# Optimization experiments

Hardware: AMD Instinct MI355X
Metric: run time of the kernel (lower is better)

The kernel has to match this reference:

```python
import jax, jax.numpy as jnp
import numpy as np

B, T, C, D, P = 8, 512, 32, 128, 1024
EPS = 1e-5

def setup_inputs() -> dict:
    key = jax.random.key(0)
    ks = jax.random.split(key, 11)
    s = 1.0 / np.sqrt(D)
    inp = {
        'x': jax.random.normal(ks[0], (B, T, C, D), jnp.float32),
        'x_mask': jax.random.randint(ks[1], (B, T, C), 0, 2) == 1,
        'p_mask': jax.random.randint(ks[2], (B, T, C), 0, 2) == 1,
        'pos': jax.random.randint(ks[3], (B, T, C), 0, P),
        'pe': jax.random.normal(ks[4], (P, D // 2, 2), jnp.float32),  # complex rpe as [re, im]
        'imp': jax.random.randint(ks[5], (B, T), 0, C),
        'idx_c': jax.random.randint(ks[6], (B, T, C), 0, C),
        'wq_w': jax.random.normal(ks[7], (D, D), jnp.float32) * s,
        'wq_b': jnp.zeros((D,), jnp.float32),
        'wk_w': jax.random.normal(ks[8], (D, D), jnp.float32) * s,
        'wk_b': jnp.zeros((D,), jnp.float32),
        'wv_w': jax.random.normal(ks[9], (D, D), jnp.float32) * s,
        'wv_b': jnp.zeros((D,), jnp.float32),
        'ls_gamma': 1e-5 * jnp.ones((D,), jnp.float32),
        'ln_gamma': jnp.ones((D,), jnp.float32),
        'ln_beta': jnp.zeros((D,), jnp.float32),
    }
    return inp


def _rotate(z, r):
    # z: (b,t,c,d) real; r: (b,t,c,d/2,2) complex multiplier [re,im]
    b, t, c, d = z.shape
    zr = z.reshape(b, t, c, d // 2, 2)
    re = zr[..., 0] * r[..., 0] - zr[..., 1] * r[..., 1]
    im = zr[..., 0] * r[..., 1] + zr[..., 1] * r[..., 0]
    return jnp.stack([re, im], axis=-1).reshape(b, t, c, d)


def reference(x, x_mask, p_mask, pos, pe, imp, idx_c,
              wq_w, wq_b, wk_w, wk_b, wv_w, wv_b,
              ls_gamma, ln_gamma, ln_beta):
    b, t, c, d = x.shape
    # channel selection gather: where x_mask, use per-token important channel
    imp_rep = jnp.broadcast_to(imp[:, :, None], (b, t, c))
    idx = jnp.where(x_mask, imp_rep, idx_c)            # (b,t,c)
    xg = jnp.take_along_axis(x, idx[..., None], axis=2)  # (b,t,c,d)
    # QKV projections (torch Linear: x @ W.T + b)
    q = xg @ wq_w.T + wq_b
    k = xg @ wk_w.T + wk_b
    v = xg @ wv_w.T + wv_b
    # relative PE complex rotation on q,k
    r = pe[pos]                                        # (b,t,c,d/2,2)
    q = _rotate(q, r)
    k = _rotate(k, r)
    # (b,c,t,d) layout; channel acts as head
    qt = q.transpose(0, 2, 1, 3)
    kt = k.transpose(0, 2, 1, 3)
    vt = v.transpose(0, 2, 1, 3)
    scores = jnp.einsum('bcqd,bckd->bcqk', qt, kt) / jnp.sqrt(jnp.float32(d))
    pm = p_mask.transpose(0, 2, 1)                     # (b,c,t)
    mask = pm[:, :, :, None] | pm[:, :, None, :]       # (b,c,t,t)
    attn = jax.nn.softmax(jnp.where(mask, -jnp.inf, scores), axis=-1)
    attn = jnp.nan_to_num(attn)
    xm = x_mask.transpose(0, 2, 1)                     # (b,c,t)
    weight = jnp.where(xm, 1.0 / t, 1.0)
    out = jnp.einsum('bcmn,bcnd->bmcd', attn * weight[:, :, None, :], vt)  # (b,t,c,d)
    # norm_first=False: LN(x + layer_scale(out))
    y = x + ls_gamma * out
    mu = jnp.mean(y, axis=-1, keepdims=True)
    var = jnp.mean(jnp.square(y - mu), axis=-1, keepdims=True)
    return (y - mu) / jnp.sqrt(var + EPS) * ln_gamma + ln_beta
```

## Files before the change

kernel.cpp:

```cpp
#include <hip/hip_runtime.h>
#include <hip/hip_bf16.h>

#define Bb 8
#define Tt 512
#define Cc 32
#define Dd 128
#define SCALE 0.08838834764831845f
#define SROW 520

typedef unsigned int u32;
typedef __hip_bfloat16 bf16;
typedef __attribute__((ext_vector_type(8))) short short8;
typedef __attribute__((ext_vector_type(4))) short short4v;
typedef __attribute__((ext_vector_type(4))) float floatx4;

__device__ __forceinline__ short f2bf(float f) {
    __hip_bfloat16 h = __float2bfloat16(f);
    return *(short*)&h;
}
__device__ __forceinline__ float bf2f(short s) {
    return __uint_as_float(((u32)(unsigned short)s) << 16);
}

__global__ __launch_bounds__(256)
void k_wconv(const float* __restrict__ wq, const float* __restrict__ wk,
             const float* __restrict__ wv, short* __restrict__ Wb)
{
    int g = blockIdx.x * 256 + threadIdx.x;
    int mat = g >> 14, rem = g & 16383;
    const float* src = (mat == 0) ? wq : (mat == 1) ? wk : wv;
    Wb[g] = f2bf(src[rem]);
}

__global__ __launch_bounds__(256)
void k_qkvm(const float* __restrict__ x, const int* __restrict__ xm,
            const int* __restrict__ pos, const float* __restrict__ pe,
            const int* __restrict__ imp, const int* __restrict__ idxc,
            const short* __restrict__ Wb,
            const float* __restrict__ bq, const float* __restrict__ bk,
            const float* __restrict__ bv,
            short* __restrict__ qb, short* __restrict__ kb, short* __restrict__ vb)
{
    const int R0  = blockIdx.x * 64;
    const int b   = R0 >> 14;
    const int t0  = (R0 >> 5) & 511;
    const int tid = threadIdx.x;
    const int w    = tid >> 6;
    const int lane = tid & 63;
    const int quad = lane >> 4;
    const int m    = lane & 15;

    __shared__ short xg[64 * 136];
    __shared__ short ot[64 * 392];

#pragma unroll
    for (int i = 0; i < 8; ++i) {
        int u   = tid + i * 256;
        int row = u >> 5, seg = u & 31;
        int R   = R0 + row;
        int idx = xm[R] ? imp[R >> 5] : idxc[R];
        float4 v = *(const float4*)(x + ((long)(R >> 5) * Cc + idx) * Dd + seg * 4);
        short4v s = {f2bf(v.x), f2bf(v.y), f2bf(v.z), f2bf(v.w)};
        *(short4v*)&xg[row * 136 + seg * 4] = s;
    }

    short8 wf[6][4];
    float  bias_v[6];
#pragma unroll
    for (int mat = 0; mat < 3; ++mat) {
        const float* bp = (mat == 0) ? bq : (mat == 1) ? bk : bv;
#pragma unroll
        for (int h = 0; h < 2; ++h) {
            int sl = mat * 2 + h;
            int ct = h * 4 + w;
            bias_v[sl] = bp[ct * 16 + m];
#pragma unroll
            for (int kb = 0; kb < 4; ++kb)
                wf[sl][kb] = *(const short8*)(Wb + ((long)mat * 128 + ct * 16 + m) * 128
                                              + kb * 32 + quad * 8);
        }
    }
    __syncthreads();

    for (int rt = 0; rt < 4; ++rt) {
        short8 af[4];
#pragma unroll
        for (int kb = 0; kb < 4; ++kb)
            af[kb] = *(const short8*)&xg[(rt * 16 + m) * 136 + kb * 32 + quad * 8];

        floatx4 acc[6];
#pragma unroll
        for (int sl = 0; sl < 6; ++sl) acc[sl] = (floatx4){0.f, 0.f, 0.f, 0.f};
#pragma unroll
        for (int kb = 0; kb < 4; ++kb)
#pragma unroll
            for (int sl = 0; sl < 6; ++sl)
                acc[sl] = __builtin_amdgcn_mfma_f32_16x16x32_bf16(af[kb], wf[sl][kb], acc[sl], 0, 0, 0);

        int po[4];
#pragma unroll
        for (int r = 0; r < 4; ++r) po[r] = pos[R0 + rt * 16 + quad * 4 + r];

#pragma unroll
        for (int sl = 0; sl < 6; ++sl) {
            int mat = sl >> 1;
            int ct  = (sl & 1) * 4 + w;
            int d   = ct * 16 + m;
#pragma unroll
            for (int r = 0; r < 4; ++r) {
                float v = acc[sl][r] + bias_v[sl];
                float p = __shfl_xor(v, 1, 64);
                if (mat < 2) {
                    const float* rp = pe + ((long)po[r] * (Dd / 2) + (d >> 1)) * 2;
                    float r0 = rp[0], r1 = rp[1];
                    v = (d & 1) ? fmaf(p, r1, v * r0) : fmaf(v, r0, -(p * r1));
                    if (mat == 0) v *= SCALE;
                }
                ot[(rt * 16 + quad * 4 + r) * 392 + mat * 128 + d] = f2bf(v);
            }
        }
    }
    __syncthreads();

    short* const mats[3] = {qb, kb, vb};
#pragma unroll
    for (int mat = 0; mat < 3; ++mat) {
        short* dst = mats[mat];
#pragma unroll
        for (int i = 0; i < 4; ++i) {
            int g = tid + i * 256;
            int n = g >> 4, off = (g & 15) * 8;
            int c = n & 31, tl = n >> 5;
            *(short8*)(dst + (((long)(b * Cc + c) * Tt) + t0 + tl) * Dd + off) =
                *(const short8*)&ot[n * 392 + mat * 128 + off];
        }
    }
}

__global__ __launch_bounds__(256)
void k_vt(const short* __restrict__ vb, const int* __restrict__ xm,
          short* __restrict__ vt)
{
    const int head = blockIdx.y;
    const int b    = head >> 5;
    const int c    = head & 31;
    const int t0   = blockIdx.x * 64;
    const int tid  = threadIdx.x;

    __shared__ short tile[64 * 136];
    __shared__ float wks[64];

    if (tid < 64)
        wks[tid] = xm[((long)b * Tt + t0 + tid) * Cc + c] ? (1.0f / Tt) : 1.0f;

    const short* src = vb + ((long)head * Tt + t0) * Dd;
#pragma unroll
    for (int i = 0; i < 4; ++i) {
        int u = tid + i * 256;
        int row = u >> 4, col = (u & 15) * 8;
        *(short8*)&tile[row * 136 + col] = *(const short8*)(src + row * Dd + col);
    }
    __syncthreads();

    short* dst = vt + (long)head * Dd * Tt + t0;
#pragma unroll
    for (int i = 0; i < 4; ++i) {
        int u = tid + i * 256;
        int d = u >> 3, t8 = (u & 7) * 8;
        short8 v;
#pragma unroll
        for (int j = 0; j < 8; ++j)
            v[j] = f2bf(bf2f(tile[(t8 + j) * 136 + d]) * wks[t8 + j]);
        *(short8*)(dst + (long)d * Tt + t8) = v;
    }
}

__global__ __launch_bounds__(512, 4)
void k_attn(const short* __restrict__ qb, const short* __restrict__ kbp,
            const short* __restrict__ vtp, const float* __restrict__ x,
            const int* __restrict__ pm,
            const float* __restrict__ lsg, const float* __restrict__ lng,
            const float* __restrict__ lnb, float* __restrict__ out)
{
    const int head = blockIdx.x;
    const int b    = head >> 5;
    const int c    = head & 31;
    const int qt0  = blockIdx.y * 64;
    const int tid  = threadIdx.x;
    const int w    = tid >> 6;
    const int lane = tid & 63;
    const int quad = lane >> 4;
    const int m    = lane & 15;

    __shared__ short S[64 * SROW];
    __shared__ u32   pkbits[16];
    __shared__ float rlS[64];
    __shared__ float ps1[8][64];
    __shared__ float ps2[8][64];
    __shared__ float mrs[64][2];

    {
        bool v = pm[((long)b * Tt + tid) * Cc + c] != 0;
        unsigned long long bal = __ballot(v);
        if (lane == 0) {
            pkbits[w * 2]     = (u32)bal;
            pkbits[w * 2 + 1] = (u32)(bal >> 32);
        }
    }

    short8 qf[4][4];
#pragma unroll
    for (int qt = 0; qt < 4; ++qt)
#pragma unroll
        for (int kb = 0; kb < 4; ++kb)
            qf[qt][kb] = *(const short8*)(qb + ((long)head * Tt + qt0 + qt * 16 + m) * Dd
                                          + kb * 32 + quad * 8);
    __syncthreads();

    for (int ch = 0; ch < 4; ++ch) {
        int kt = ch * 128 + w * 16 + m;
        const short* kp = kbp + ((long)head * Tt + kt) * Dd + quad * 8;
        floatx4 sc[4];
#pragma unroll
        for (int qt = 0; qt < 4; ++qt) sc[qt] = (floatx4){0.f, 0.f, 0.f, 0.f};
#pragma unroll
        for (int kb = 0; kb < 4; ++kb) {
            short8 bk = *(const short8*)(kp + kb * 32);
#pragma unroll
            for (int qt = 0; qt < 4; ++qt)
                sc[qt] = __builtin_amdgcn_mfma_f32_16x16x32_bf16(qf[qt][kb], bk, sc[qt], 0, 0, 0);
        }
        bool masked = (pkbits[kt >> 5] >> (kt & 31)) & 1;
#pragma unroll
        for (int qt = 0; qt < 4; ++qt)
#pragma unroll
            for (int r = 0; r < 4; ++r)
                S[(qt * 16 + quad * 4 + r) * SROW + kt] = f2bf(masked ? -1e30f : sc[qt][r]);
    }
    __syncthreads();

    {
        int qi = tid >> 3, part = tid & 7;
        short* rowp = &S[qi * SROW + part * 64];
        short8 sv[8];
#pragma unroll
        for (int j = 0; j < 8; ++j) sv[j] = *(short8*)&rowp[j * 8];
        float mx = -1e30f;
#pragma unroll
        for (int j = 0; j < 8; ++j)
#pragma unroll
            for (int e = 0; e < 8; ++e) mx = fmaxf(mx, bf2f(sv[j][e]));
        mx = fmaxf(mx, __shfl_xor(mx, 1, 64));
        mx = fmaxf(mx, __shfl_xor(mx, 2, 64));
        mx = fmaxf(mx, __shfl_xor(mx, 4, 64));
        float l = 0.f;
#pragma unroll
        for (int j = 0; j < 8; ++j)
#pragma unroll
            for (int e = 0; e < 8; ++e) {
                float s = bf2f(sv[j][e]);
                float ex = (s <= -1e29f) ? 0.f : __expf(s - mx);
                sv[j][e] = f2bf(ex);
                l += ex;
            }
#pragma unroll
        for (int j = 0; j < 8; ++j) *(short8*)&rowp[j * 8] = sv[j];
        l += __shfl_xor(l, 1, 64);
        l += __shfl_xor(l, 2, 64);
        l += __shfl_xor(l, 4, 64);
        if (part == 0) {
            int t = qt0 + qi;
            bool qmask = (pkbits[t >> 5] >> (t & 31)) & 1;
            rlS[qi] = (l > 0.f && !qmask) ? 1.0f / l : 0.f;
        }
    }
    __syncthreads();

    floatx4 oa[4];
#pragma unroll
    for (int qt = 0; qt < 4; ++qt) oa[qt] = (floatx4){0.f, 0.f, 0.f, 0.f};

    const short* vbase = vtp + (long)head * Dd * Tt + ((long)(w * 16 + m)) * Tt + quad * 8;
    for (int kv = 0; kv < 16; ++kv) {
        short8 bv = *(const short8*)(vbase + kv * 32);
#pragma unroll
        for (int qt = 0; qt < 4; ++qt) {
            short8 ap = *(const short8*)&S[(qt * 16 + m) * SROW + kv * 32 + quad * 8];
            oa[qt] = __builtin_amdgcn_mfma_f32_16x16x32_bf16(ap, bv, oa[qt], 0, 0, 0);
        }
    }

    const int d = w * 16 + m;
    const float lg = lsg[d];
    float yv[4][4];
    float s1[4][4], s2[4][4];
#pragma unroll
    for (int qt = 0; qt < 4; ++qt)
#pragma unroll
        for (int r = 0; r < 4; ++r) {
            int row = qt * 16 + quad * 4 + r;
            int t = qt0 + row;
            float val = oa[qt][r] * rlS[row];
            float y = x[(((long)b * Tt + t) * Cc + c) * Dd + d] + lg * val;
            yv[qt][r] = y;
            s1[qt][r] = y;
            s2[qt][r] = y * y;
        }
#pragma unroll
    for (int qt = 0; qt < 4; ++qt)
#pragma unroll
        for (int r = 0; r < 4; ++r) {
            float a = s1[qt][r], bb = s2[qt][r];
            a += __shfl_xor(a, 1, 64); bb += __shfl_xor(bb, 1, 64);
            a += __shfl_xor(a, 2, 64); bb += __shfl_xor(bb, 2, 64);
            a += __shfl_xor(a, 4, 64); bb += __shfl_xor(bb, 4, 64);
            a += __shfl_xor(a, 8, 64); bb += __shfl_xor(bb, 8, 64);
            if (m == 0) {
                ps1[w][qt * 16 + quad * 4 + r] = a;
                ps2[w][qt * 16 + quad * 4 + r] = bb;
            }
        }
    __syncthreads();
    if (tid < 64) {
        float a = 0.f, bb = 0.f;
#pragma unroll
        for (int wv = 0; wv < 8; ++wv) { a += ps1[wv][tid]; bb += ps2[wv][tid]; }
        float mean = a * (1.0f / Dd);
        float var  = bb * (1.0f / Dd) - mean * mean;
        mrs[tid][0] = mean;
        mrs[tid][1] = rsqrtf(var + 1e-5f);
    }
    __syncthreads();

    const float g = lng[d], be = lnb[d];
#pragma unroll
    for (int qt = 0; qt < 4; ++qt)
#pragma unroll
        for (int r = 0; r < 4; ++r) {
            int row = qt * 16 + quad * 4 + r;
            int t = qt0 + row;
            out[(((long)b * Tt + t) * Cc + c) * Dd + d] =
                (yv[qt][r] - mrs[row][0]) * mrs[row][1] * g + be;
        }
}

extern "C" void kernel_launch(void* const* d_in, const int* in_sizes, int n_in,
                              void* d_out, int out_size, void* d_ws, size_t ws_size,
                              hipStream_t stream) {
    const float* x    = (const float*)d_in[0];
    const int* xmask  = (const int*)d_in[1];
    const int* pmask  = (const int*)d_in[2];
    const int* pos    = (const int*)d_in[3];
    const float* pe   = (const float*)d_in[4];
    const int* imp    = (const int*)d_in[5];
    const int* idxc   = (const int*)d_in[6];
    const float* wq_w = (const float*)d_in[7];
    const float* wq_b = (const float*)d_in[8];
    const float* wk_w = (const float*)d_in[9];
    const float* wk_b = (const float*)d_in[10];
    const float* wv_w = (const float*)d_in[11];
    const float* wv_b = (const float*)d_in[12];
    const float* lsg  = (const float*)d_in[13];
    const float* lng  = (const float*)d_in[14];
    const float* lnb  = (const float*)d_in[15];
    float* out = (float*)d_out;

    size_t n = (size_t)Bb * Cc * Tt * Dd;
    short* qb = (short*)d_ws;
    short* kb = qb + n;
    short* vb = kb + n;
    short* vt = vb + n;
    short* Wb = vt + n;

    k_wconv<<<dim3(3 * Dd * Dd / 256), dim3(256), 0, stream>>>(wq_w, wk_w, wv_w, Wb);
    k_qkvm<<<dim3(Bb * Tt * Cc / 64), dim3(256), 0, stream>>>(
        x, xmask, pos, pe, imp, idxc, Wb, wq_b, wk_b, wv_b, qb, kb, vb);
    k_vt<<<dim3(Tt / 64, Bb * Cc), dim3(256), 0, stream>>>(vb, xmask, vt);
    k_attn<<<dim3(Bb * Cc, Tt / 64), dim3(512), 0, stream>>>(
        qb, kb, vt, x, pmask, lsg, lng, lnb, out);
}
```

Measured before the change: 330.1 us.

## Fuse V transpose into QKV kernel, swizzle LDS, remap attention blocks per XCD

The QKV kernel now tiles by (head, 64 tokens) instead of 64 consecutive rows. This lets it apply the x_mask weight to V and write the transposed V directly, so the separate k_vt kernel and the intermediate vb buffer are gone. The shared-memory output tile uses an XOR swizzle to cut bank conflicts on both the row-wise writes and the transposed reads. The attention grid is remapped so that blocks of the same head land on the same XCD for L2 reuse, and the softmax row reads are interleaved across threads. In exchange, the gather of x in the QKV kernel is now strided across channels, which may make those loads less coalesced.

```diff
diff --git a/kernel.cpp b/kernel.cpp
--- a/kernel.cpp
+++ b/kernel.cpp
@@ -39,12 +39,13 @@
             const short* __restrict__ Wb,
             const float* __restrict__ bq, const float* __restrict__ bk,
             const float* __restrict__ bv,
-            short* __restrict__ qb, short* __restrict__ kb, short* __restrict__ vb)
+            short* __restrict__ qb, short* __restrict__ kb, short* __restrict__ vt)
 {
-    const int R0  = blockIdx.x * 64;
-    const int b   = R0 >> 14;
-    const int t0  = (R0 >> 5) & 511;
-    const int tid = threadIdx.x;
+    const int t0   = blockIdx.x * 64;
+    const int head = blockIdx.y;
+    const int b    = head >> 5;
+    const int c    = head & 31;
+    const int tid  = threadIdx.x;
     const int w    = tid >> 6;
     const int lane = tid & 63;
     const int quad = lane >> 4;
@@ -52,16 +53,20 @@
 
     __shared__ short xg[64 * 136];
     __shared__ short ot[64 * 392];
+    __shared__ float wks[64];
 
 #pragma unroll
     for (int i = 0; i < 8; ++i) {
         int u   = tid + i * 256;
         int row = u >> 5, seg = u & 31;
-        int R   = R0 + row;
-        int idx = xm[R] ? imp[R >> 5] : idxc[R];
-        float4 v = *(const float4*)(x + ((long)(R >> 5) * Cc + idx) * Dd + seg * 4);
+        long tr = (long)(b * Tt + t0 + row);
+        long R  = tr * Cc + c;
+        int xmv = xm[R];
+        int idx = xmv ? imp[tr] : idxc[R];
+        float4 v = *(const float4*)(x + (tr * Cc + idx) * Dd + seg * 4);
         short4v s = {f2bf(v.x), f2bf(v.y), f2bf(v.z), f2bf(v.w)};
         *(short4v*)&xg[row * 136 + seg * 4] = s;
+        if (seg == 0) wks[row] = xmv ? (1.0f / Tt) : 1.0f;
     }
 
     short8 wf[6][4];
@@ -75,9 +80,9 @@
             int ct = h * 4 + w;
             bias_v[sl] = bp[ct * 16 + m];
 #pragma unroll
-            for (int kb = 0; kb < 4; ++kb)
-                wf[sl][kb] = *(const short8*)(Wb + ((long)mat * 128 + ct * 16 + m) * 128
-                                              + kb * 32 + quad * 8);
+            for (int kk = 0; kk < 4; ++kk)
+                wf[sl][kk] = *(const short8*)(Wb + ((long)mat * 128 + ct * 16 + m) * 128
+                                              + kk * 32 + quad * 8);
         }
     }
     __syncthreads();
@@ -85,21 +90,22 @@
     for (int rt = 0; rt < 4; ++rt) {
         short8 af[4];
 #pragma unroll
-        for (int kb = 0; kb < 4; ++kb)
-            af[kb] = *(const short8*)&xg[(rt * 16 + m) * 136 + kb * 32 + quad * 8];
+        for (int kk = 0; kk < 4; ++kk)
+            af[kk] = *(const short8*)&xg[(rt * 16 + m) * 136 + kk * 32 + quad * 8];
 
         floatx4 acc[6];
 #pragma unroll
         for (int sl = 0; sl < 6; ++sl) acc[sl] = (floatx4){0.f, 0.f, 0.f, 0.f};
 #pragma unroll
-        for (int kb = 0; kb < 4; ++kb)
+        for (int kk = 0; kk < 4; ++kk)
 #pragma unroll
             for (int sl = 0; sl < 6; ++sl)
-                acc[sl] = __builtin_amdgcn_mfma_f32_16x16x32_bf16(af[kb], wf[sl][kb], acc[sl], 0, 0, 0);
+                acc[sl] = __builtin_amdgcn_mfma_f32_16x16x32_bf16(af[kk], wf[sl][kk], acc[sl], 0, 0, 0);
 
         int po[4];
 #pragma unroll
-        for (int r = 0; r < 4; ++r) po[r] = pos[R0 + rt * 16 + quad * 4 + r];
+        for (int r = 0; r < 4; ++r)
+            po[r] = pos[((long)(b * Tt + t0 + rt * 16 + quad * 4 + r)) * Cc + c];
 
 #pragma unroll
         for (int sl = 0; sl < 6; ++sl) {
@@ -110,68 +116,44 @@
             for (int r = 0; r < 4; ++r) {
                 float v = acc[sl][r] + bias_v[sl];
                 float p = __shfl_xor(v, 1, 64);
+                int row = rt * 16 + quad * 4 + r;
                 if (mat < 2) {
                     const float* rp = pe + ((long)po[r] * (Dd / 2) + (d >> 1)) * 2;
                     float r0 = rp[0], r1 = rp[1];
                     v = (d & 1) ? fmaf(p, r1, v * r0) : fmaf(v, r0, -(p * r1));
                     if (mat == 0) v *= SCALE;
+                } else {
+                    v *= wks[row];
                 }
-                ot[(rt * 16 + quad * 4 + r) * 392 + mat * 128 + d] = f2bf(v);
+                int e = mat * 128 + d;
+                ot[row * 392 + (e ^ (((row >> 3) & 7) << 3))] = f2bf(v);
             }
         }
     }
     __syncthreads();
 
-    short* const mats[3] = {qb, kb, vb};
-#pragma unroll
-    for (int mat = 0; mat < 3; ++mat) {
-        short* dst = mats[mat];
+    short* const mats2[2] = {qb, kb};
+#pragma unroll
+    for (int mat = 0; mat < 2; ++mat) {
+        short* dst = mats2[mat];
 #pragma unroll
         for (int i = 0; i < 4; ++i) {
             int g = tid + i * 256;
             int n = g >> 4, off = (g & 15) * 8;
-            int c = n & 31, tl = n >> 5;
-            *(short8*)(dst + (((long)(b * Cc + c) * Tt) + t0 + tl) * Dd + off) =
-                *(const short8*)&ot[n * 392 + mat * 128 + off];
-        }
-    }
-}
-
-__global__ __launch_bounds__(256)
-void k_vt(const short* __restrict__ vb, const int* __restrict__ xm,
-          short* __restrict__ vt)
-{
-    const int head = blockIdx.y;
-    const int b    = head >> 5;
-    const int c    = head & 31;
-    const int t0   = blockIdx.x * 64;
-    const int tid  = threadIdx.x;
-
-    __shared__ short tile[64 * 136];
-    __shared__ float wks[64];
-
-    if (tid < 64)
-        wks[tid] = xm[((long)b * Tt + t0 + tid) * Cc + c] ? (1.0f / Tt) : 1.0f;
-
-    const short* src = vb + ((long)head * Tt + t0) * Dd;
-#pragma unroll
-    for (int i = 0; i < 4; ++i) {
-        int u = tid + i * 256;
-        int row = u >> 4, col = (u & 15) * 8;
-        *(short8*)&tile[row * 136 + col] = *(const short8*)(src + row * Dd + col);
-    }
-    __syncthreads();
-
-    short* dst = vt + (long)head * Dd * Tt + t0;
+            *(short8*)(dst + ((long)head * Tt + t0 + n) * Dd + off) =
+                *(const short8*)&ot[n * 392 + mat * 128 + (off ^ (((n >> 3) & 7) << 3))];
+        }
+    }
 #pragma unroll
     for (int i = 0; i < 4; ++i) {
         int u = tid + i * 256;
         int d = u >> 3, t8 = (u & 7) * 8;
+        int key = (u & 7) << 3;
         short8 v;
 #pragma unroll
         for (int j = 0; j < 8; ++j)
-            v[j] = f2bf(bf2f(tile[(t8 + j) * 136 + d]) * wks[t8 + j]);
-        *(short8*)(dst + (long)d * Tt + t8) = v;
+            v[j] = ot[(t8 + j) * 392 + 256 + (d ^ key)];
+        *(short8*)(vt + ((long)head * Dd + d) * Tt + t0 + t8) = v;
     }
 }
 
@@ -182,10 +164,16 @@
             const float* __restrict__ lsg, const float* __restrict__ lng,
             const float* __restrict__ lnb, float* __restrict__ out)
 {
-    const int head = blockIdx.x;
+    const int l    = blockIdx.y * 256 + blockIdx.x;
+    const int xcd  = l & 7;
+    const int sws  = l >> 3;
+    const int hh   = sws & 7;
+    const int tl   = (sws >> 3) & 7;
+    const int gg   = sws >> 6;
+    const int head = xcd + ((gg * 8 + hh) << 3);
     const int b    = head >> 5;
     const int c    = head & 31;
-    const int qt0  = blockIdx.y * 64;
+    const int qt0  = tl * 64;
     const int tid  = threadIdx.x;
     const int w    = tid >> 6;
     const int lane = tid & 63;
@@ -212,9 +200,9 @@
 #pragma unroll
     for (int qt = 0; qt < 4; ++qt)
 #pragma unroll
-        for (int kb = 0; kb < 4; ++kb)
-            qf[qt][kb] = *(const short8*)(qb + ((long)head * Tt + qt0 + qt * 16 + m) * Dd
-                                          + kb * 32 + quad * 8);
+        for (int kk = 0; kk < 4; ++kk)
+            qf[qt][kk] = *(const short8*)(qb + ((long)head * Tt + qt0 + qt * 16 + m) * Dd
+                                          + kk * 32 + quad * 8);
     __syncthreads();
 
     for (int ch = 0; ch < 4; ++ch) {
@@ -224,11 +212,11 @@
 #pragma unroll
         for (int qt = 0; qt < 4; ++qt) sc[qt] = (floatx4){0.f, 0.f, 0.f, 0.f};
 #pragma unroll
-        for (int kb = 0; kb < 4; ++kb) {
-            short8 bk = *(const short8*)(kp + kb * 32);
+        for (int kk = 0; kk < 4; ++kk) {
+            short8 bk = *(const short8*)(kp + kk * 32);
 #pragma unroll
             for (int qt = 0; qt < 4; ++qt)
-                sc[qt] = __builtin_amdgcn_mfma_f32_16x16x32_bf16(qf[qt][kb], bk, sc[qt], 0, 0, 0);
+                sc[qt] = __builtin_amdgcn_mfma_f32_16x16x32_bf16(qf[qt][kk], bk, sc[qt], 0, 0, 0);
         }
         bool masked = (pkbits[kt >> 5] >> (kt & 31)) & 1;
 #pragma unroll
@@ -241,10 +229,10 @@
 
     {
         int qi = tid >> 3, part = tid & 7;
-        short* rowp = &S[qi * SROW + part * 64];
+        short* rowp = &S[qi * SROW + part * 8];
         short8 sv[8];
 #pragma unroll
-        for (int j = 0; j < 8; ++j) sv[j] = *(short8*)&rowp[j * 8];
+        for (int j = 0; j < 8; ++j) sv[j] = *(short8*)&rowp[j * 64];
         float mx = -1e30f;
 #pragma unroll
         for (int j = 0; j < 8; ++j)
@@ -253,7 +241,7 @@
         mx = fmaxf(mx, __shfl_xor(mx, 1, 64));
         mx = fmaxf(mx, __shfl_xor(mx, 2, 64));
         mx = fmaxf(mx, __shfl_xor(mx, 4, 64));
-        float l = 0.f;
+        float lsum = 0.f;
 #pragma unroll
         for (int j = 0; j < 8; ++j)
 #pragma unroll
@@ -261,17 +249,17 @@
                 float s = bf2f(sv[j][e]);
                 float ex = (s <= -1e29f) ? 0.f : __expf(s - mx);
                 sv[j][e] = f2bf(ex);
-                l += ex;
+                lsum += ex;
             }
 #pragma unroll
-        for (int j = 0; j < 8; ++j) *(short8*)&rowp[j * 8] = sv[j];
-        l += __shfl_xor(l, 1, 64);
-        l += __shfl_xor(l, 2, 64);
-        l += __shfl_xor(l, 4, 64);
+        for (int j = 0; j < 8; ++j) *(short8*)&rowp[j * 64] = sv[j];
+        lsum += __shfl_xor(lsum, 1, 64);
+        lsum += __shfl_xor(lsum, 2, 64);
+        lsum += __shfl_xor(lsum, 4, 64);
         if (part == 0) {
             int t = qt0 + qi;
             bool qmask = (pkbits[t >> 5] >> (t & 31)) & 1;
-            rlS[qi] = (l > 0.f && !qmask) ? 1.0f / l : 0.f;
+            rlS[qi] = (lsum > 0.f && !qmask) ? 1.0f / lsum : 0.f;
         }
     }
     __syncthreads();
@@ -368,14 +356,12 @@
     size_t n = (size_t)Bb * Cc * Tt * Dd;
     short* qb = (short*)d_ws;
     short* kb = qb + n;
-    short* vb = kb + n;
-    short* vt = vb + n;
+    short* vt = kb + n;
     short* Wb = vt + n;
 
     k_wconv<<<dim3(3 * Dd * Dd / 256), dim3(256), 0, stream>>>(wq_w, wk_w, wv_w, Wb);
-    k_qkvm<<<dim3(Bb * Tt * Cc / 64), dim3(256), 0, stream>>>(
-        x, xmask, pos, pe, imp, idxc, Wb, wq_b, wk_b, wv_b, qb, kb, vb);
-    k_vt<<<dim3(Tt / 64, Bb * Cc), dim3(256), 0, stream>>>(vb, xmask, vt);
-    k_attn<<<dim3(Bb * Cc, Tt / 64), dim3(512), 0, stream>>>(
+    k_qkvm<<<dim3(Tt / 64, Bb * Cc), dim3(256), 0, stream>>>(
+        x, xmask, pos, pe, imp, idxc, Wb, wq_b, wk_b, wv_b, qb, kb, vt);
+    k_attn<<<dim3(256, Tt / 64), dim3(512), 0, stream>>>(
         qb, kb, vt, x, pmask, lsg, lng, lnb, out);
 }
```

Result: slower. 340.6 us (+3.2%).

## Halve attention query tile and remap blocks for XCD-local head grouping

Applied to the files above, without the earlier changes.

The attention kernel now handles 32 query rows per block instead of 64, which halves the shared score buffer and the per-thread register arrays so more blocks can be resident (launch bounds raised to 8). The block index is also remapped so blocks sharing a head land on the same XCD, with the aim of improving L2 reuse of K and V. The softmax pass is reorganised to 16 threads per row with strided reads. The cost is twice as many blocks, each reloading the full K/V and the padding mask, which adds global traffic per query row.

```diff
diff --git a/kernel.cpp b/kernel.cpp
--- a/kernel.cpp
+++ b/kernel.cpp
@@ -75,9 +75,9 @@
             int ct = h * 4 + w;
             bias_v[sl] = bp[ct * 16 + m];
 #pragma unroll
-            for (int kb = 0; kb < 4; ++kb)
-                wf[sl][kb] = *(const short8*)(Wb + ((long)mat * 128 + ct * 16 + m) * 128
-                                              + kb * 32 + quad * 8);
+            for (int kk = 0; kk < 4; ++kk)
+                wf[sl][kk] = *(const short8*)(Wb + ((long)mat * 128 + ct * 16 + m) * 128
+                                              + kk * 32 + quad * 8);
         }
     }
     __syncthreads();
@@ -85,17 +85,17 @@
     for (int rt = 0; rt < 4; ++rt) {
         short8 af[4];
 #pragma unroll
-        for (int kb = 0; kb < 4; ++kb)
-            af[kb] = *(const short8*)&xg[(rt * 16 + m) * 136 + kb * 32 + quad * 8];
+        for (int kk = 0; kk < 4; ++kk)
+            af[kk] = *(const short8*)&xg[(rt * 16 + m) * 136 + kk * 32 + quad * 8];
 
         floatx4 acc[6];
 #pragma unroll
         for (int sl = 0; sl < 6; ++sl) acc[sl] = (floatx4){0.f, 0.f, 0.f, 0.f};
 #pragma unroll
-        for (int kb = 0; kb < 4; ++kb)
+        for (int kk = 0; kk < 4; ++kk)
 #pragma unroll
             for (int sl = 0; sl < 6; ++sl)
-                acc[sl] = __builtin_amdgcn_mfma_f32_16x16x32_bf16(af[kb], wf[sl][kb], acc[sl], 0, 0, 0);
+                acc[sl] = __builtin_amdgcn_mfma_f32_16x16x32_bf16(af[kk], wf[sl][kk], acc[sl], 0, 0, 0);
 
         int po[4];
 #pragma unroll
@@ -175,29 +175,35 @@
     }
 }
 
-__global__ __launch_bounds__(512, 4)
+__global__ __launch_bounds__(512, 8)
 void k_attn(const short* __restrict__ qb, const short* __restrict__ kbp,
             const short* __restrict__ vtp, const float* __restrict__ x,
             const int* __restrict__ pm,
             const float* __restrict__ lsg, const float* __restrict__ lng,
             const float* __restrict__ lnb, float* __restrict__ out)
 {
-    const int head = blockIdx.x;
+    const int l    = blockIdx.y * 256 + blockIdx.x;
+    const int xcd  = l & 7;
+    const int sws  = l >> 3;
+    const int hh   = sws & 7;
+    const int tl   = (sws >> 3) & 15;
+    const int gg   = sws >> 7;
+    const int head = xcd + ((gg * 8 + hh) << 3);
     const int b    = head >> 5;
     const int c    = head & 31;
-    const int qt0  = blockIdx.y * 64;
+    const int qt0  = tl * 32;
     const int tid  = threadIdx.x;
     const int w    = tid >> 6;
     const int lane = tid & 63;
     const int quad = lane >> 4;
     const int m    = lane & 15;
 
-    __shared__ short S[64 * SROW];
+    __shared__ short S[32 * SROW];
     __shared__ u32   pkbits[16];
-    __shared__ float rlS[64];
-    __shared__ float ps1[8][64];
-    __shared__ float ps2[8][64];
-    __shared__ float mrs[64][2];
+    __shared__ float rlS[32];
+    __shared__ float ps1[8][32];
+    __shared__ float ps2[8][32];
+    __shared__ float mrs[32][2];
 
     {
         bool v = pm[((long)b * Tt + tid) * Cc + c] != 0;
@@ -208,31 +214,31 @@
         }
     }
 
-    short8 qf[4][4];
-#pragma unroll
-    for (int qt = 0; qt < 4; ++qt)
-#pragma unroll
-        for (int kb = 0; kb < 4; ++kb)
-            qf[qt][kb] = *(const short8*)(qb + ((long)head * Tt + qt0 + qt * 16 + m) * Dd
-                                          + kb * 32 + quad * 8);
+    short8 qf[2][4];
+#pragma unroll
+    for (int qt = 0; qt < 2; ++qt)
+#pragma unroll
+        for (int kk = 0; kk < 4; ++kk)
+            qf[qt][kk] = *(const short8*)(qb + ((long)head * Tt + qt0 + qt * 16 + m) * Dd
+                                          + kk * 32 + quad * 8);
     __syncthreads();
 
     for (int ch = 0; ch < 4; ++ch) {
         int kt = ch * 128 + w * 16 + m;
         const short* kp = kbp + ((long)head * Tt + kt) * Dd + quad * 8;
-        floatx4 sc[4];
-#pragma unroll
-        for (int qt = 0; qt < 4; ++qt) sc[qt] = (floatx4){0.f, 0.f, 0.f, 0.f};
-#pragma unroll
-        for (int kb = 0; kb < 4; ++kb) {
-            short8 bk = *(const short8*)(kp + kb * 32);
-#pragma unroll
-            for (int qt = 0; qt < 4; ++qt)
-                sc[qt] = __builtin_amdgcn_mfma_f32_16x16x32_bf16(qf[qt][kb], bk, sc[qt], 0, 0, 0);
+        floatx4 sc[2];
+#pragma unroll
+        for (int qt = 0; qt < 2; ++qt) sc[qt] = (floatx4){0.f, 0.f, 0.f, 0.f};
+#pragma unroll
+        for (int kk = 0; kk < 4; ++kk) {
+            short8 bk = *(const short8*)(kp + kk * 32);
+#pragma unroll
+            for (int qt = 0; qt < 2; ++qt)
+                sc[qt] = __builtin_amdgcn_mfma_f32_16x16x32_bf16(qf[qt][kk], bk, sc[qt], 0, 0, 0);
         }
         bool masked = (pkbits[kt >> 5] >> (kt & 31)) & 1;
 #pragma unroll
-        for (int qt = 0; qt < 4; ++qt)
+        for (int qt = 0; qt < 2; ++qt)
 #pragma unroll
             for (int r = 0; r < 4; ++r)
                 S[(qt * 16 + quad * 4 + r) * SROW + kt] = f2bf(masked ? -1e30f : sc[qt][r]);
@@ -240,51 +246,53 @@
     __syncthreads();
 
     {
-        int qi = tid >> 3, part = tid & 7;
-        short* rowp = &S[qi * SROW + part * 64];
-        short8 sv[8];
-#pragma unroll
-        for (int j = 0; j < 8; ++j) sv[j] = *(short8*)&rowp[j * 8];
+        int qi = tid >> 4, part = tid & 15;
+        short* rowp = &S[qi * SROW + part * 8];
+        short8 sv[4];
+#pragma unroll
+        for (int j = 0; j < 4; ++j) sv[j] = *(short8*)&rowp[j * 128];
         float mx = -1e30f;
 #pragma unroll
-        for (int j = 0; j < 8; ++j)
+        for (int j = 0; j < 4; ++j)
 #pragma unroll
             for (int e = 0; e < 8; ++e) mx = fmaxf(mx, bf2f(sv[j][e]));
         mx = fmaxf(mx, __shfl_xor(mx, 1, 64));
         mx = fmaxf(mx, __shfl_xor(mx, 2, 64));
         mx = fmaxf(mx, __shfl_xor(mx, 4, 64));
-        float l = 0.f;
-#pragma unroll
-        for (int j = 0; j < 8; ++j)
+        mx = fmaxf(mx, __shfl_xor(mx, 8, 64));
+        float lsum = 0.f;
+#pragma unroll
+        for (int j = 0; j < 4; ++j)
 #pragma unroll
             for (int e = 0; e < 8; ++e) {
                 float s = bf2f(sv[j][e]);
                 float ex = (s <= -1e29f) ? 0.f : __expf(s - mx);
                 sv[j][e] = f2bf(ex);
-                l += ex;
+                lsum += ex;
             }
 #pragma unroll
-        for (int j = 0; j < 8; ++j) *(short8*)&rowp[j * 8] = sv[j];
-        l += __shfl_xor(l, 1, 64);
-        l += __shfl_xor(l, 2, 64);
-        l += __shfl_xor(l, 4, 64);
+        for (int j = 0; j < 4; ++j) *(short8*)&rowp[j * 128] = sv[j];
+        lsum += __shfl_xor(lsum, 1, 64);
+        lsum += __shfl_xor(lsum, 2, 64);
+        lsum += __shfl_xor(lsum, 4, 64);
+        lsum += __shfl_xor(lsum, 8, 64);
         if (part == 0) {
             int t = qt0 + qi;
             bool qmask = (pkbits[t >> 5] >> (t & 31)) & 1;
-            rlS[qi] = (l > 0.f && !qmask) ? 1.0f / l : 0.f;
-        }
-    }
-    __syncthreads();
-
-    floatx4 oa[4];
-#pragma unroll
-    for (int qt = 0; qt < 4; ++qt) oa[qt] = (floatx4){0.f, 0.f, 0.f, 0.f};
+            rlS[qi] = (lsum > 0.f && !qmask) ? 1.0f / lsum : 0.f;
+        }
+    }
+    __syncthreads();
+
+    floatx4 oa[2];
+#pragma unroll
+    for (int qt = 0; qt < 2; ++qt) oa[qt] = (floatx4){0.f, 0.f, 0.f, 0.f};
 
     const short* vbase = vtp + (long)head * Dd * Tt + ((long)(w * 16 + m)) * Tt + quad * 8;
     for (int kv = 0; kv < 16; ++kv) {
         short8 bv = *(const short8*)(vbase + kv * 32);
 #pragma unroll
-        for (int qt = 0; qt < 4; ++qt) {
+        for (int qt = 0; qt < 2; ++qt) {
             short8 ap = *(const short8*)&S[(qt * 16 + m) * SROW + kv * 32 + quad * 8];
             oa[qt] = __builtin_amdgcn_mfma_f32_16x16x32_bf16(ap, bv, oa[qt], 0, 0, 0);
         }
@@ -292,10 +300,10 @@
 
     const int d = w * 16 + m;
     const float lg = lsg[d];
-    float yv[4][4];
-    float s1[4][4], s2[4][4];
-#pragma unroll
-    for (int qt = 0; qt < 4; ++qt)
+    float yv[2][4];
+    float s1[2][4], s2[2][4];
+#pragma unroll
+    for (int qt = 0; qt < 2; ++qt)
 #pragma unroll
         for (int r = 0; r < 4; ++r) {
             int row = qt * 16 + quad * 4 + r;
@@ -307,7 +315,7 @@
             s2[qt][r] = y * y;
         }
 #pragma unroll
-    for (int qt = 0; qt < 4; ++qt)
+    for (int qt = 0; qt < 2; ++qt)
 #pragma unroll
         for (int r = 0; r < 4; ++r) {
             float a = s1[qt][r], bb = s2[qt][r];
@@ -321,7 +329,7 @@
             }
         }
     __syncthreads();
-    if (tid < 64) {
+    if (tid < 32) {
         float a = 0.f, bb = 0.f;
 #pragma unroll
         for (int wv = 0; wv < 8; ++wv) { a += ps1[wv][tid]; bb += ps2[wv][tid]; }
@@ -334,7 +342,7 @@
 
     const float g = lng[d], be = lnb[d];
 #pragma unroll
-    for (int qt = 0; qt < 4; ++qt)
+    for (int qt = 0; qt < 2; ++qt)
 #pragma unroll
         for (int r = 0; r < 4; ++r) {
             int row = qt * 16 + quad * 4 + r;
@@ -376,6 +384,6 @@
     k_qkvm<<<dim3(Bb * Tt * Cc / 64), dim3(256), 0, stream>>>(
         x, xmask, pos, pe, imp, idxc, Wb, wq_b, wk_b, wv_b, qb, kb, vb);
     k_vt<<<dim3(Tt / 64, Bb * Cc), dim3(256), 0, stream>>>(vb, xmask, vt);
-    k_attn<<<dim3(Bb * Cc, Tt / 64), dim3(512), 0, stream>>>(
+    k_attn<<<dim3(256, Tt / 16 / 2), dim3(512), 0, stream>>>(
         qb, kb, vt, x, pmask, lsg, lng, lnb, out);
 }
```

Measured after the change: 380.7 us. 1.15x slower.

## Remap attention blocks per XCD, prefetch V and x, add MFMA priority hints

Applied to the files above, without the earlier changes.

The attention kernel now flattens its grid and remaps block ids so that the 8 query tiles of a head land on the same XCD, improving L2 reuse of K and V. V fragments and residual x values are loaded before the softmax barrier and double-buffered through the PV loop, hiding global-load latency behind the softmax and MFMA work. s_setprio is raised around the MFMA bursts, and the softmax row access is changed to an interleaved stride to reduce LDS bank conflicts. Holding the prefetched data raises register pressure, which could lower occupancy under the 512x4 launch bound.

```diff
diff --git a/kernel.cpp b/kernel.cpp
--- a/kernel.cpp
+++ b/kernel.cpp
@@ -75,9 +75,9 @@
             int ct = h * 4 + w;
             bias_v[sl] = bp[ct * 16 + m];
 #pragma unroll
-            for (int kb = 0; kb < 4; ++kb)
-                wf[sl][kb] = *(const short8*)(Wb + ((long)mat * 128 + ct * 16 + m) * 128
-                                              + kb * 32 + quad * 8);
+            for (int kk = 0; kk < 4; ++kk)
+                wf[sl][kk] = *(const short8*)(Wb + ((long)mat * 128 + ct * 16 + m) * 128
+                                              + kk * 32 + quad * 8);
         }
     }
     __syncthreads();
@@ -85,17 +85,17 @@
     for (int rt = 0; rt < 4; ++rt) {
         short8 af[4];
 #pragma unroll
-        for (int kb = 0; kb < 4; ++kb)
-            af[kb] = *(const short8*)&xg[(rt * 16 + m) * 136 + kb * 32 + quad * 8];
+        for (int kk = 0; kk < 4; ++kk)
+            af[kk] = *(const short8*)&xg[(rt * 16 + m) * 136 + kk * 32 + quad * 8];
 
         floatx4 acc[6];
 #pragma unroll
         for (int sl = 0; sl < 6; ++sl) acc[sl] = (floatx4){0.f, 0.f, 0.f, 0.f};
 #pragma unroll
-        for (int kb = 0; kb < 4; ++kb)
+        for (int kk = 0; kk < 4; ++kk)
 #pragma unroll
             for (int sl = 0; sl < 6; ++sl)
-                acc[sl] = __builtin_amdgcn_mfma_f32_16x16x32_bf16(af[kb], wf[sl][kb], acc[sl], 0, 0, 0);
+                acc[sl] = __builtin_amdgcn_mfma_f32_16x16x32_bf16(af[kk], wf[sl][kk], acc[sl], 0, 0, 0);
 
         int po[4];
 #pragma unroll
@@ -182,15 +182,22 @@
             const float* __restrict__ lsg, const float* __restrict__ lng,
             const float* __restrict__ lnb, float* __restrict__ out)
 {
-    const int head = blockIdx.x;
+    const int l    = blockIdx.y * 256 + blockIdx.x;
+    const int xcd  = l & 7;
+    const int sws  = l >> 3;
+    const int hh   = sws & 7;
+    const int tl   = (sws >> 3) & 7;
+    const int gg   = sws >> 6;
+    const int head = xcd + ((gg * 8 + hh) << 3);
     const int b    = head >> 5;
     const int c    = head & 31;
-    const int qt0  = blockIdx.y * 64;
+    const int qt0  = tl * 64;
     const int tid  = threadIdx.x;
     const int w    = tid >> 6;
     const int lane = tid & 63;
     const int quad = lane >> 4;
     const int m    = lane & 15;
+    const int d    = w * 16 + m;
 
     __shared__ short S[64 * SROW];
     __shared__ u32   pkbits[16];
@@ -212,9 +219,9 @@
 #pragma unroll
     for (int qt = 0; qt < 4; ++qt)
 #pragma unroll
-        for (int kb = 0; kb < 4; ++kb)
-            qf[qt][kb] = *(const short8*)(qb + ((long)head * Tt + qt0 + qt * 16 + m) * Dd
-                                          + kb * 32 + quad * 8);
+        for (int kk = 0; kk < 4; ++kk)
+            qf[qt][kk] = *(const short8*)(qb + ((long)head * Tt + qt0 + qt * 16 + m) * Dd
+                                          + kk * 32 + quad * 8);
     __syncthreads();
 
     for (int ch = 0; ch < 4; ++ch) {
@@ -224,11 +231,13 @@
 #pragma unroll
         for (int qt = 0; qt < 4; ++qt) sc[qt] = (floatx4){0.f, 0.f, 0.f, 0.f};
 #pragma unroll
-        for (int kb = 0; kb < 4; ++kb) {
-            short8 bk = *(const short8*)(kp + kb * 32);
+        for (int kk = 0; kk < 4; ++kk) {
+            short8 bk = *(const short8*)(kp + kk * 32);
+            __builtin_amdgcn_s_setprio(1);
 #pragma unroll
             for (int qt = 0; qt < 4; ++qt)
-                sc[qt] = __builtin_amdgcn_mfma_f32_16x16x32_bf16(qf[qt][kb], bk, sc[qt], 0, 0, 0);
+                sc[qt] = __builtin_amdgcn_mfma_f32_16x16x32_bf16(qf[qt][kk], bk, sc[qt], 0, 0, 0);
+            __builtin_amdgcn_s_setprio(0);
         }
         bool masked = (pkbits[kt >> 5] >> (kt & 31)) & 1;
 #pragma unroll
@@ -237,14 +246,29 @@
             for (int r = 0; r < 4; ++r)
                 S[(qt * 16 + quad * 4 + r) * SROW + kt] = f2bf(masked ? -1e30f : sc[qt][r]);
     }
+
+    const short* vbase = vtp + (long)head * Dd * Tt + ((long)d) * Tt + quad * 8;
+    short8 bvbuf[8];
+#pragma unroll
+    for (int kv = 0; kv < 8; ++kv)
+        bvbuf[kv] = *(const short8*)(vbase + kv * 32);
+
+    float xv[4][4];
+#pragma unroll
+    for (int qt = 0; qt < 4; ++qt)
+#pragma unroll
+        for (int r = 0; r < 4; ++r) {
+            int row = qt * 16 + quad * 4 + r;
+            xv[qt][r] = x[(((long)b * Tt + qt0 + row) * Cc + c) * Dd + d];
+        }
     __syncthreads();
 
     {
         int qi = tid >> 3, part = tid & 7;
-        short* rowp = &S[qi * SROW + part * 64];
+        short* rowp = &S[qi * SROW + part * 8];
         short8 sv[8];
 #pragma unroll
-        for (int j = 0; j < 8; ++j) sv[j] = *(short8*)&rowp[j * 8];
+        for (int j = 0; j < 8; ++j) sv[j] = *(short8*)&rowp[j * 64];
         float mx = -1e30f;
 #pragma unroll
         for (int j = 0; j < 8; ++j)
@@ -253,7 +277,7 @@
         mx = fmaxf(mx, __shfl_xor(mx, 1, 64));
         mx = fmaxf(mx, __shfl_xor(mx, 2, 64));
         mx = fmaxf(mx, __shfl_xor(mx, 4, 64));
-        float l = 0.f;
+        float lsum = 0.f;
 #pragma unroll
         for (int j = 0; j < 8; ++j)
 #pragma unroll
@@ -261,17 +285,17 @@
                 float s = bf2f(sv[j][e]);
                 float ex = (s <= -1e29f) ? 0.f : __expf(s - mx);
                 sv[j][e] = f2bf(ex);
-                l += ex;
+                lsum += ex;
             }
 #pragma unroll
-        for (int j = 0; j < 8; ++j) *(short8*)&rowp[j * 8] = sv[j];
-        l += __shfl_xor(l, 1, 64);
-        l += __shfl_xor(l, 2, 64);
-        l += __shfl_xor(l, 4, 64);
+        for (int j = 0; j < 8; ++j) *(short8*)&rowp[j * 64] = sv[j];
+        lsum += __shfl_xor(lsum, 1, 64);
+        lsum += __shfl_xor(lsum, 2, 64);
+        lsum += __shfl_xor(lsum, 4, 64);
         if (part == 0) {
             int t = qt0 + qi;
             bool qmask = (pkbits[t >> 5] >> (t & 31)) & 1;
-            rlS[qi] = (l > 0.f && !qmask) ? 1.0f / l : 0.f;
+            rlS[qi] = (lsum > 0.f && !qmask) ? 1.0f / lsum : 0.f;
         }
     }
     __syncthreads();
@@ -280,37 +304,35 @@
 #pragma unroll
     for (int qt = 0; qt < 4; ++qt) oa[qt] = (floatx4){0.f, 0.f, 0.f, 0.f};
 
-    const short* vbase = vtp + (long)head * Dd * Tt + ((long)(w * 16 + m)) * Tt + quad * 8;
+#pragma unroll
     for (int kv = 0; kv < 16; ++kv) {
-        short8 bv = *(const short8*)(vbase + kv * 32);
+        short8 bv = bvbuf[kv & 7];
+        if (kv < 8) bvbuf[kv] = *(const short8*)(vbase + (kv + 8) * 32);
+        __builtin_amdgcn_s_setprio(1);
 #pragma unroll
         for (int qt = 0; qt < 4; ++qt) {
             short8 ap = *(const short8*)&S[(qt * 16 + m) * SROW + kv * 32 + quad * 8];
             oa[qt] = __builtin_amdgcn_mfma_f32_16x16x32_bf16(ap, bv, oa[qt], 0, 0, 0);
         }
-    }
-
-    const int d = w * 16 + m;
+        __builtin_amdgcn_s_setprio(0);
+    }
+
     const float lg = lsg[d];
     float yv[4][4];
-    float s1[4][4], s2[4][4];
 #pragma unroll
     for (int qt = 0; qt < 4; ++qt)
 #pragma unroll
         for (int r = 0; r < 4; ++r) {
             int row = qt * 16 + quad * 4 + r;
-            int t = qt0 + row;
             float val = oa[qt][r] * rlS[row];
-            float y = x[(((long)b * Tt + t) * Cc + c) * Dd + d] + lg * val;
+            float y = xv[qt][r] + lg * val;
             yv[qt][r] = y;
-            s1[qt][r] = y;
-            s2[qt][r] = y * y;
         }
 #pragma unroll
     for (int qt = 0; qt < 4; ++qt)
 #pragma unroll
         for (int r = 0; r < 4; ++r) {
-            float a = s1[qt][r], bb = s2[qt][r];
+            float a = yv[qt][r], bb = yv[qt][r] * yv[qt][r];
             a += __shfl_xor(a, 1, 64); bb += __shfl_xor(bb, 1, 64);
             a += __shfl_xor(a, 2, 64); bb += __shfl_xor(bb, 2, 64);
             a += __shfl_xor(a, 4, 64); bb += __shfl_xor(bb, 4, 64);
@@ -376,6 +398,6 @@
     k_qkvm<<<dim3(Bb * Tt * Cc / 64), dim3(256), 0, stream>>>(
         x, xmask, pos, pe, imp, idxc, Wb, wq_b, wk_b, wv_b, qb, kb, vb);
     k_vt<<<dim3(Tt / 64, Bb * Cc), dim3(256), 0, stream>>>(vb, xmask, vt);
-    k_attn<<<dim3(Bb * Cc, Tt / 64), dim3(512), 0, stream>>>(
+    k_attn<<<dim3(256, 8), dim3(512), 0, stream>>>(
         qb, kb, vt, x, pmask, lsg, lng, lnb, out);
 }
```

After: 346.7 us. +5.0%, slower.
